# Kernel optimization log

Hardware: AMD Instinct MI355X
Metric: run time of the kernel (lower is better)

## Reference

```python
import jax, jax.numpy as jnp
import numpy as np

B, S, D, E, H, K = 2, 2048, 1024, 8, 2048, 2
EM_ITERS = 5
LB_WEIGHT = 0.1
EPS = 1e-8


def setup_inputs() -> dict:
    key = jax.random.key(0)
    ks = jax.random.split(key, 12)
    sc = 0.02
    return {
        "x": jax.random.normal(ks[0], (B, S, D), jnp.float32),
        "gate_W": jax.random.normal(ks[1], (D, E), jnp.float32) * sc,
        "gate_b": jnp.zeros((E,), jnp.float32),
        "gate_temp": jnp.ones((1,), jnp.float32),
        "W1": jax.random.normal(ks[2], (E, D, H), jnp.float32) * sc,
        "b1": jnp.zeros((E, H), jnp.float32),
        "W2": jax.random.normal(ks[3], (E, H, D), jnp.float32) * sc,
        "b2": jnp.zeros((E, D), jnp.float32),
        "sW1": jax.random.normal(ks[4], (D, H), jnp.float32) * sc,
        "sb1": jnp.zeros((H,), jnp.float32),
        "sW2": jax.random.normal(ks[5], (H, D), jnp.float32) * sc,
        "sb2": jnp.zeros((D,), jnp.float32),
    }


def reference(x, gate_W, gate_b, gate_temp, W1, b1, W2, b2, sW1, sb1, sW2, sb2):
    Bq, Sq, Dq = x.shape
    T = Bq * Sq
    xf = x.reshape(T, Dq)  # (T, D)

    # Router: gate linear + learned temperature
    gate_logits = xf @ gate_W + gate_b              # (T, E)
    tempered = gate_logits / gate_temp               # (T, E)
    expert_weights = jax.nn.softmax(tempered, axis=-1)
    _, topk_idx = jax.lax.top_k(expert_weights, K)   # (T, K) int32
    first = topk_idx[:, 0]

    # Load-balance loss: KL(uniform || empirical top-1 usage) (fresh counters)
    usage = jnp.zeros((E,), jnp.float32).at[first].add(1.0)
    actual = usage / jnp.float32(T)
    actual = actual + EPS
    actual = actual / actual.sum()
    u = jnp.float32(1.0 / E)
    kl = jnp.sum(u * (jnp.log(u) - jnp.log(actual)))
    load_balance_loss = LB_WEIGHT * kl

    # EM expert-load reweighting on tempered logits
    scores = jax.nn.softmax(tempered, axis=-1)       # (T, E)
    p = jnp.full((E,), 1.0 / E, jnp.float32)
    for _ in range(EM_ITERS):
        ea = scores * p                               # (T, E)
        ea = ea / (ea.sum(axis=-1, keepdims=True) + EPS)
        counts = ea.sum(axis=0)                       # (E,)
        p = counts / (counts.sum() + EPS)
    balanced = scores * p                             # (T, E)

    # All-expert FFN (dense, equivalent to per-expert masked compute)
    h = jax.nn.relu(jnp.einsum('td,edh->teh', xf, W1) + b1)  # (T, E, H)
    eo = jnp.einsum('teh,ehd->ted', h, W2) + b2              # (T, E, D)

    # Combine top-k experts with balanced weights
    w_k = jnp.take_along_axis(balanced, topk_idx, axis=1)        # (T, K)
    out_k = jnp.take_along_axis(eo, topk_idx[:, :, None], axis=1)  # (T, K, D)
    out = jnp.einsum('tk,tkd->td', w_k, out_k)                   # (T, D)

    # Shared expert, weighted by 0.1
    shared = jax.nn.relu(xf @ sW1 + sb1) @ sW2 + sb2
    out = out + 0.1 * shared

    return out.reshape(Bq, Sq, Dq), load_balance_loss
```

## Files before the change

kernel.cpp:

```cpp
#include <hip/hip_runtime.h>
#include <math.h>

#define T_TOK 4096
#define D_DIM 1024
#define H_DIM 2048
#define NE 8
#define EPSF 1e-8f
#define G1_GEMM 448
#define G2_GEMM 224
#define NTR128 1152

typedef __attribute__((ext_vector_type(8))) short bf16x8;
typedef __attribute__((ext_vector_type(4))) float f32x4;

__device__ __forceinline__ unsigned short f2bf(float f) {
  unsigned u = __float_as_uint(f);
  u += 0x7fffu + ((u >> 16) & 1u);
  return (unsigned short)(u >> 16);
}

__device__ __forceinline__ void gload_lds16(const void* g, void* l) {
  __builtin_amdgcn_global_load_lds(
      (const __attribute__((address_space(1))) unsigned int*)g,
      (__attribute__((address_space(3))) unsigned int*)l, 16, 0, 0);
}

#define WAITV(n) asm volatile("s_waitcnt vmcnt(" #n ")" ::: "memory")
#define BARR()                                  \
  do {                                          \
    asm volatile("" ::: "memory");              \
    __builtin_amdgcn_s_barrier();               \
    asm volatile("" ::: "memory");              \
  } while (0)

__device__ __forceinline__ void transpose_tile128(const float* __restrict__ src,
                                                  unsigned short* __restrict__ dst,
                                                  int R, int C, int r0, int c0, int tid,
                                                  float* tile) {
#pragma unroll
  for (int k = 0; k < 8; ++k) {
    int id = tid + k * 512;
    int row = id >> 5, c4 = (id & 31) * 4;
    float4 v = *(const float4*)(src + (size_t)(r0 + row) * C + c0 + c4);
    float* tr = tile + row * 129 + c4;
    tr[0] = v.x; tr[1] = v.y; tr[2] = v.z; tr[3] = v.w;
  }
  __syncthreads();
#pragma unroll
  for (int k = 0; k < 4; ++k) {
    int id = tid + k * 512;
    int oc = id >> 4;
    int rbase = (id & 15) * 8;
    uint4 wv;
    unsigned* wp = (unsigned*)&wv;
#pragma unroll
    for (int j = 0; j < 4; ++j) {
      unsigned lo = f2bf(tile[(rbase + 2 * j) * 129 + oc]);
      unsigned hi = f2bf(tile[(rbase + 2 * j + 1) * 129 + oc]);
      wp[j] = lo | (hi << 16);
    }
    *(uint4*)(dst + (size_t)(c0 + oc) * R + r0 + rbase) = wv;
  }
}

__global__ __launch_bounds__(512, 4) void prep2_kernel(
    const float* __restrict__ x, const float* __restrict__ gW, const float* __restrict__ gb,
    const float* __restrict__ gtemp, const float* __restrict__ W1, const float* __restrict__ sW1,
    unsigned short* __restrict__ W1t, unsigned short* __restrict__ sW1t,
    unsigned short* __restrict__ xb, float* __restrict__ scores, int* __restrict__ idx,
    unsigned* __restrict__ usage, unsigned* __restrict__ cnt, int* __restrict__ perm) {
  __shared__ char psm[67584];
  int b = blockIdx.x, tid = threadIdx.x;
  if (b >= 512) {
    int l = b - 512;
    int m = l >> 7, rem = l & 127;
    int c0 = (rem & 15) * 128, r0 = (rem >> 4) * 128;
    const float* src = (m < NE) ? W1 + (size_t)m * D_DIM * H_DIM : sW1;
    unsigned short* dst = (m < NE) ? W1t + (size_t)m * D_DIM * H_DIM : sW1t;
    transpose_tile128(src, dst, D_DIM, H_DIM, r0, c0, tid, (float*)psm);
    return;
  }
  float* gWl = (float*)psm;
  int* toks = (int*)(psm + 36864);
  int wave = tid >> 6, lane = tid & 63;
  int t0 = b * 8;
#pragma unroll
  for (int k = 0; k < 4; ++k) {
    int q = tid + k * 512;
    float4 f = ((const float4*)gW)[q];
    int d = q >> 1, eo = (q & 1) * 4;
    float* dstv = &gWl[d * 9 + eo];
    dstv[0] = f.x; dstv[1] = f.y; dstv[2] = f.z; dstv[3] = f.w;
  }
  __syncthreads();
  int t = t0 + wave;
  const float* xr = x + (size_t)t * D_DIM;
  unsigned short* xbr = xb + (size_t)t * D_DIM;
  float part[NE];
#pragma unroll
  for (int e = 0; e < NE; ++e) part[e] = 0.f;
#pragma unroll
  for (int i = 0; i < 16; ++i) {
    int d = lane + 64 * i;
    float xv = xr[d];
    xbr[d] = f2bf(xv);
    const float* g = &gWl[d * 9];
#pragma unroll
    for (int e = 0; e < NE; ++e) part[e] += xv * g[e];
  }
#pragma unroll
  for (int e = 0; e < NE; ++e) {
    float v = part[e];
    for (int off = 32; off; off >>= 1) v += __shfl_xor(v, off);
    part[e] = v;
  }
  float temp = gtemp[0];
  float mx = -1e30f;
#pragma unroll
  for (int e = 0; e < NE; ++e) { part[e] = (part[e] + gb[e]) / temp; mx = fmaxf(mx, part[e]); }
  float s = 0.f;
#pragma unroll
  for (int e = 0; e < NE; ++e) { part[e] = expf(part[e] - mx); s += part[e]; }
  float inv = 1.0f / s;
#pragma unroll
  for (int e = 0; e < NE; ++e) part[e] *= inv;
  if (lane == 0) {
    float4* sp = (float4*)(scores + (size_t)t * NE);
    sp[0] = make_float4(part[0], part[1], part[2], part[3]);
    sp[1] = make_float4(part[4], part[5], part[6], part[7]);
    int i0 = 0; float b0 = part[0];
#pragma unroll
    for (int e = 1; e < NE; ++e) if (part[e] > b0) { b0 = part[e]; i0 = e; }
    int i1 = -1; float b1 = -1e30f;
#pragma unroll
    for (int e = 0; e < NE; ++e) if (e != i0 && part[e] > b1) { b1 = part[e]; i1 = e; }
    idx[t * 2] = i0; idx[t * 2 + 1] = i1;
    toks[wave * 2] = i0; toks[wave * 2 + 1] = i1;
  }
  __syncthreads();
  if (tid < NE) {
    int c0 = 0, c1 = 0;
#pragma unroll
    for (int j = 0; j < 8; ++j) {
      if (toks[j * 2] == tid) ++c0;
      if (toks[j * 2 + 1] == tid) ++c1;
    }
    if (c0) atomicAdd(&usage[tid], (unsigned)c0);
    int tot = c0 + c1;
    if (tot) {
      unsigned bb = atomicAdd(&cnt[tid], (unsigned)tot);
      int p = 0;
#pragma unroll
      for (int j = 0; j < 8; ++j) {
        if (toks[j * 2] == tid) perm[(size_t)tid * T_TOK + bb + p++] = (t0 + j) * 2;
        if (toks[j * 2 + 1] == tid) perm[(size_t)tid * T_TOK + bb + p++] = (t0 + j) * 2 + 1;
      }
    }
  }
}

__device__ __forceinline__ void em_block512(const float* __restrict__ scores,
                                            const unsigned* __restrict__ usage,
                                            float* __restrict__ p_out, float* __restrict__ loss_out,
                                            int tid, char* smem) {
  float* p_sh = (float*)smem;
  float* cw = p_sh + 8;
  float* counts_sh = cw + 64;
  int wave = tid >> 6, lane = tid & 63;
  float s[8][NE];
#pragma unroll
  for (int rr = 0; rr < 8; ++rr) {
    int row = tid + rr * 512;
    const float4* sp = (const float4*)(scores + (size_t)row * NE);
    float4 a = sp[0], b = sp[1];
    s[rr][0] = a.x; s[rr][1] = a.y; s[rr][2] = a.z; s[rr][3] = a.w;
    s[rr][4] = b.x; s[rr][5] = b.y; s[rr][6] = b.z; s[rr][7] = b.w;
  }
  if (tid < NE) p_sh[tid] = 1.0f / NE;
  __syncthreads();
  for (int it = 0; it < 5; ++it) {
    float p[NE];
#pragma unroll
    for (int e = 0; e < NE; ++e) p[e] = p_sh[e];
    float c[NE];
#pragma unroll
    for (int e = 0; e < NE; ++e) c[e] = 0.f;
#pragma unroll
    for (int rr = 0; rr < 8; ++rr) {
      float denom = 0.f;
#pragma unroll
      for (int e = 0; e < NE; ++e) denom += s[rr][e] * p[e];
      float inv = 1.0f / (denom + EPSF);
#pragma unroll
      for (int e = 0; e < NE; ++e) c[e] += s[rr][e] * p[e] * inv;
    }
#pragma unroll
    for (int e = 0; e < NE; ++e) {
      float v = c[e];
      for (int off = 32; off; off >>= 1) v += __shfl_xor(v, off);
      c[e] = v;
    }
    if (lane == 0) {
#pragma unroll
      for (int e = 0; e < NE; ++e) cw[wave * 8 + e] = c[e];
    }
    __syncthreads();
    if (tid < NE) {
      float tot = 0.f;
#pragma unroll
      for (int w = 0; w < 8; ++w) tot += cw[w * 8 + tid];
      counts_sh[tid] = tot;
    }
    __syncthreads();
    if (tid < NE) {
      float total = 0.f;
#pragma unroll
      for (int e = 0; e < NE; ++e) total += counts_sh[e];
      p_sh[tid] = counts_sh[tid] / (total + EPSF);
    }
    __syncthreads();
  }
  if (tid < NE) p_out[tid] = p_sh[tid];
  if (tid == 0) {
    float actual[NE]; float norm = 0.f;
#pragma unroll
    for (int e = 0; e < NE; ++e) { actual[e] = (float)usage[e] / (float)T_TOK + EPSF; norm += actual[e]; }
    float u = 1.0f / NE;
    float kl = 0.f;
#pragma unroll
    for (int e = 0; e < NE; ++e) kl += u * (logf(u) - logf(actual[e] / norm));
    loss_out[0] = 0.1f * kl;
  }
}

template <int KDIM, int NDIM, bool RELU, bool MODE1>
__device__ __forceinline__ void gemm_body(
    unsigned short* lds, int flat,
    const unsigned short* __restrict__ A, const unsigned short* __restrict__ WE,
    const unsigned short* __restrict__ WS, const float* __restrict__ biasE,
    const float* __restrict__ biasS, const int* __restrict__ perm,
    const unsigned* __restrict__ cnt, void* __restrict__ outp) {
  constexpr int BM = 256, BN = 256, BK = 64;
  constexpr int NT = NDIM / BN;
  constexpr int NKT = KDIM / BK;

  int tc[9];
#pragma unroll
  for (int i = 0; i < NE; ++i) tc[i] = ((int)cnt[i] + 255) >> 8;
  tc[8] = T_TOK / 256;
  int nt = 0;
#pragma unroll
  for (int i = 0; i < 9; ++i) nt += tc[i];
  int W = nt * NT;
  int xcd = flat & 7, pos = flat >> 3;
  int q = W >> 3, r = W & 7;
  int mycount = q + (xcd < r ? 1 : 0);
  if (pos >= mycount) return;
  int mystart = xcd * q + (xcd < r ? xcd : r);
  int w = mystart + pos;
  int ti = w / NT;
  int n0 = (w % NT) * BN;
  int e = 0, mt = ti;
  while (mt >= tc[e]) { mt -= tc[e]; ++e; }
  int m0 = mt * BM;
  int cnt_e = (e == NE) ? T_TOK : (int)cnt[e];

  const unsigned short* Bmat = (e == NE) ? WS : WE + (size_t)e * KDIM * NDIM;
  const float* bias = (e == NE) ? biasS : biasE + (size_t)e * NDIM;

  int tid = threadIdx.x, wave = tid >> 6, lane = tid & 63;
  int wm = wave >> 1, wn = wave & 1;
  int frow = lane & 15, fks = lane >> 4;

  int srow = wave * 8 + (lane >> 3);
  int sslot = lane & 7;
  const unsigned short* aptr[2][2];
  const unsigned short* bptr[2][2];
#pragma unroll
  for (int h = 0; h < 2; ++h)
#pragma unroll
    for (int j = 0; j < 2; ++j) {
      int rr = h * 128 + j * 64 + srow;
      int colsw = (sslot ^ (rr & 7)) << 3;
      int ar = m0 + rr;
      if (ar > cnt_e - 1) ar = cnt_e - 1;
      int gar;
      if (e == NE) gar = MODE1 ? ar : (2 * T_TOK + ar);
      else { int v = perm[(size_t)e * T_TOK + ar]; gar = MODE1 ? (v >> 1) : v; }
      aptr[h][j] = A + (size_t)gar * KDIM + colsw;
      bptr[h][j] = Bmat + (size_t)(n0 + rr) * KDIM + colsw;
    }

  auto stA = [&](int t, int h) {
    int dbe = (t & 1) * 16384;
    int k0 = t * BK;
    gload_lds16(aptr[h][0] + k0, &lds[dbe + h * 8192 + wave * 512]);
    gload_lds16(aptr[h][1] + k0, &lds[dbe + h * 8192 + wave * 512 + 4096]);
  };
  auto stB = [&](int t, int h) {
    int dbe = (t & 1) * 16384;
    int k0 = t * BK;
    gload_lds16(bptr[h][0] + k0, &lds[32768 + dbe + h * 8192 + wave * 512]);
    gload_lds16(bptr[h][1] + k0, &lds[32768 + dbe + h * 8192 + wave * 512 + 4096]);
  };

  auto rdA = [&](int dbe, int ks, int m) -> bf16x8 {
    int rr = wm * 64 + m * 16 + frow;
    int slot = (ks * 4 + fks) ^ (rr & 7);
    return *(const bf16x8*)&lds[dbe + rr * 64 + slot * 8];
  };
  auto rdB = [&](int dbe, int ks, int bh, int jj) -> bf16x8 {
    int rr = bh * 128 + jj * 32 + wn * 16 + frow;
    int slot = (ks * 4 + fks) ^ (rr & 7);
    return *(const bf16x8*)&lds[32768 + dbe + rr * 64 + slot * 8];
  };

  f32x4 acc[4][8];
#pragma unroll
  for (int m = 0; m < 4; ++m)
#pragma unroll
    for (int nn = 0; nn < 8; ++nn) acc[m][nn] = (f32x4){0.f, 0.f, 0.f, 0.f};

  stA(0, 0); stA(0, 1);
  stB(0, 0); stB(0, 1);
  stA(1, 0); stA(1, 1);
  WAITV(4);
  BARR();

  for (int t = 0; t < NKT; ++t) {
    const int dbe = (t & 1) * 16384;
    bf16x8 a0[4], a1[4], b0[4], b1[4];

#pragma unroll
    for (int m = 0; m < 4; ++m) a0[m] = rdA(dbe, 0, m);
#pragma unroll
    for (int m = 0; m < 4; ++m) a1[m] = rdA(dbe, 1, m);
#pragma unroll
    for (int jj = 0; jj < 4; ++jj) b0[jj] = rdB(dbe, 0, 0, jj);
#pragma unroll
    for (int jj = 0; jj < 4; ++jj) b1[jj] = rdB(dbe, 1, 0, jj);
    if (t + 1 < NKT) { stB(t + 1, 0); stB(t + 1, 1); }
    BARR();
    __builtin_amdgcn_s_setprio(1);
#pragma unroll
    for (int m = 0; m < 4; ++m)
#pragma unroll
      for (int jj = 0; jj < 4; ++jj)
        acc[m][jj] = __builtin_amdgcn_mfma_f32_16x16x32_bf16(a0[m], b0[jj], acc[m][jj], 0, 0, 0);
#pragma unroll
    for (int m = 0; m < 4; ++m)
#pragma unroll
      for (int jj = 0; jj < 4; ++jj)
        acc[m][jj] = __builtin_amdgcn_mfma_f32_16x16x32_bf16(a1[m], b1[jj], acc[m][jj], 0, 0, 0);
    __builtin_amdgcn_s_setprio(0);
    BARR();

#pragma unroll
    for (int jj = 0; jj < 4; ++jj) b0[jj] = rdB(dbe, 0, 1, jj);
#pragma unroll
    for (int jj = 0; jj < 4; ++jj) b1[jj] = rdB(dbe, 1, 1, jj);
    if (t + 2 < NKT) { stA(t + 2, 0); stA(t + 2, 1); }
    BARR();
    __builtin_amdgcn_s_setprio(1);
#pragma unroll
    for (int m = 0; m < 4; ++m)
#pragma unroll
      for (int jj = 0; jj < 4; ++jj)
        acc[m][4 + jj] = __builtin_amdgcn_mfma_f32_16x16x32_bf16(a0[m], b0[jj], acc[m][4 + jj], 0, 0, 0);
#pragma unroll
    for (int m = 0; m < 4; ++m)
#pragma unroll
      for (int jj = 0; jj < 4; ++jj)
        acc[m][4 + jj] = __builtin_amdgcn_mfma_f32_16x16x32_bf16(a1[m], b1[jj], acc[m][4 + jj], 0, 0, 0);
    __builtin_amdgcn_s_setprio(0);
    if (t + 2 < NKT) { WAITV(4); }
    else if (t + 1 < NKT) { WAITV(0); }
    BARR();
  }

#pragma unroll
  for (int m = 0; m < 4; ++m) {
#pragma unroll
    for (int qq = 0; qq < 4; ++qq) {
      int rt = wm * 64 + m * 16 + (lane >> 4) * 4 + qq;
      if (m0 + rt >= cnt_e) continue;
      int rr;
      if (e == NE) rr = 2 * T_TOK + m0 + rt;
      else rr = perm[(size_t)e * T_TOK + m0 + rt];
#pragma unroll
      for (int nn = 0; nn < 8; ++nn) {
        int col = n0 + (nn >> 2) * 128 + (nn & 3) * 32 + wn * 16 + (lane & 15);
        float val = acc[m][nn][qq] + bias[col];
        if (RELU) val = fmaxf(val, 0.f);
        if (MODE1)
          ((unsigned short*)outp)[(size_t)rr * NDIM + col] = f2bf(val);
        else
          ((float*)outp)[(size_t)rr * NDIM + col] = val;
      }
    }
  }
}

__global__ __launch_bounds__(512, 2) void gemm1_kernel(
    const unsigned short* __restrict__ xb, const unsigned short* __restrict__ W1t,
    const unsigned short* __restrict__ sW1t, const float* __restrict__ b1,
    const float* __restrict__ sb1, const int* __restrict__ perm, const unsigned* __restrict__ cnt,
    unsigned short* __restrict__ Hbuf,
    const float* __restrict__ W2, const float* __restrict__ sW2,
    unsigned short* __restrict__ W2t, unsigned short* __restrict__ sW2t,
    const float* __restrict__ scores, const unsigned* __restrict__ usage,
    float* __restrict__ pbuf, float* __restrict__ loss_out) {
  __shared__ char smem[131072];
  int flat = blockIdx.x;
  if (flat < G1_GEMM) {
    gemm_body<D_DIM, H_DIM, true, true>((unsigned short*)smem, flat, xb, W1t, sW1t, b1, sb1,
                                        perm, cnt, (void*)Hbuf);
    return;
  }
  int l = flat - G1_GEMM;
  if (l < NTR128) {
    int m = l >> 7, rem = l & 127;
    int c0 = (rem & 7) * 128, r0 = (rem >> 3) * 128;
    const float* src = (m < NE) ? W2 + (size_t)m * H_DIM * D_DIM : sW2;
    unsigned short* dst = (m < NE) ? W2t + (size_t)m * H_DIM * D_DIM : sW2t;
    transpose_tile128(src, dst, H_DIM, D_DIM, r0, c0, threadIdx.x, (float*)smem);
    return;
  }
  em_block512(scores, usage, pbuf, loss_out, threadIdx.x, smem);
}

template <int KDIM, int NDIM, bool RELU, bool MODE1>
__global__ __launch_bounds__(512, 2) void gemm_kernel(
    const unsigned short* __restrict__ A, const unsigned short* __restrict__ WE,
    const unsigned short* __restrict__ WS, const float* __restrict__ biasE,
    const float* __restrict__ biasS, const int* __restrict__ perm,
    const unsigned* __restrict__ cnt, void* __restrict__ outp) {
  __shared__ char smem[131072];
  gemm_body<KDIM, NDIM, RELU, MODE1>((unsigned short*)smem, blockIdx.x, A, WE, WS, biasE, biasS,
                                     perm, cnt, outp);
}

__global__ void combine_kernel(const float* __restrict__ ebuf, const float* __restrict__ scores,
                               const float* __restrict__ p, const int* __restrict__ idx,
                               float* __restrict__ out) {
  int gid = blockIdx.x * blockDim.x + threadIdx.x;
  int t = gid >> 8;
  int d4 = gid & 255;
  int e0 = idx[t * 2], e1 = idx[t * 2 + 1];
  float w0 = scores[(size_t)t * NE + e0] * p[e0];
  float w1 = scores[(size_t)t * NE + e1] * p[e1];
  const float4* r0 = (const float4*)(ebuf + (size_t)(t * 2) * D_DIM);
  const float4* r1 = (const float4*)(ebuf + (size_t)(t * 2 + 1) * D_DIM);
  const float4* rs = (const float4*)(ebuf + (size_t)(2 * T_TOK + t) * D_DIM);
  float4 a = r0[d4], b = r1[d4], c = rs[d4];
  float4 o;
  o.x = w0 * a.x + w1 * b.x + 0.1f * c.x;
  o.y = w0 * a.y + w1 * b.y + 0.1f * c.y;
  o.z = w0 * a.z + w1 * b.z + 0.1f * c.z;
  o.w = w0 * a.w + w1 * b.w + 0.1f * c.w;
  ((float4*)out)[gid] = o;
}

extern "C" void kernel_launch(void* const* d_in, const int* in_sizes, int n_in,
                              void* d_out, int out_size, void* d_ws, size_t ws_size,
                              hipStream_t stream) {
  const float* x     = (const float*)d_in[0];
  const float* gW    = (const float*)d_in[1];
  const float* gb    = (const float*)d_in[2];
  const float* gtemp = (const float*)d_in[3];
  const float* W1    = (const float*)d_in[4];
  const float* b1    = (const float*)d_in[5];
  const float* W2    = (const float*)d_in[6];
  const float* b2    = (const float*)d_in[7];
  const float* sW1   = (const float*)d_in[8];
  const float* sb1   = (const float*)d_in[9];
  const float* sW2   = (const float*)d_in[10];
  const float* sb2   = (const float*)d_in[11];
  float* out = (float*)d_out;

  char* ws = (char*)d_ws;
  size_t off = 0;
  auto take = [&](size_t b) { char* ptr = ws + off; off += (b + 255) & ~(size_t)255; return ptr; };
  unsigned short* xb   = (unsigned short*)take((size_t)T_TOK * D_DIM * 2);
  unsigned short* W1t  = (unsigned short*)take((size_t)NE * H_DIM * D_DIM * 2);
  unsigned short* sW1t = (unsigned short*)take((size_t)H_DIM * D_DIM * 2);
  unsigned short* W2t  = (unsigned short*)take((size_t)NE * D_DIM * H_DIM * 2);
  unsigned short* sW2t = (unsigned short*)take((size_t)D_DIM * H_DIM * 2);
  unsigned short* Hbuf = (unsigned short*)take((size_t)3 * T_TOK * H_DIM * 2);
  float* ebuf          = (float*)take((size_t)3 * T_TOK * D_DIM * 4);
  float* scores        = (float*)take((size_t)T_TOK * NE * 4);
  int* idx             = (int*)take((size_t)T_TOK * 2 * 4);
  int* perm            = (int*)take((size_t)NE * T_TOK * 4);
  unsigned* cnt        = (unsigned*)take(256);
  unsigned* usage      = (unsigned*)take(256);
  float* pbuf          = (float*)take(256);
  (void)n_in; (void)in_sizes; (void)out_size; (void)ws_size;

  hipMemsetAsync(cnt, 0, 512, stream);
  prep2_kernel<<<512 + NTR128, 512, 0, stream>>>(x, gW, gb, gtemp, W1, sW1, W1t, sW1t, xb,
                                                 scores, idx, usage, cnt, perm);
  gemm1_kernel<<<G1_GEMM + NTR128 + 1, 512, 0, stream>>>(
      xb, W1t, sW1t, b1, sb1, perm, cnt, Hbuf, W2, sW2, W2t, sW2t, scores, usage, pbuf,
      out + (size_t)T_TOK * D_DIM);
  gemm_kernel<H_DIM, D_DIM, false, false><<<G2_GEMM, 512, 0, stream>>>(
      Hbuf, W2t, sW2t, b2, sb2, perm, cnt, (void*)ebuf);
  combine_kernel<<<(T_TOK * D_DIM / 4) / 256, 256, 0, stream>>>(ebuf, scores, pbuf, idx, out);
}
```

Before: 196.3 us.

## Fuse MoE pipeline into persistent ticketed megakernel with fine-grained dataflow sync

```diff
diff --git a/kernel.cpp b/kernel.cpp
--- a/kernel.cpp
+++ b/kernel.cpp
@@ -6,9 +6,26 @@
 #define H_DIM 2048
 #define NE 8
 #define EPSF 1e-8f
-#define G1_GEMM 448
-#define G2_GEMM 224
-#define NTR128 1152
+
+#define NT1 8
+#define NT2 4
+#define OFF_W1 512
+#define N_W1 1152
+#define OFF_G1 (OFF_W1 + N_W1)
+#define N_G1 448
+#define OFF_W2 (OFF_G1 + N_G1)
+#define N_W2 1152
+#define OFF_EM (OFF_W2 + N_W2)
+#define OFF_G2 (OFF_EM + 1)
+#define N_G2 448
+#define N_TICKETS (OFF_G2 + N_G2)
+#define HROWS 14336
+
+#define S_Q 0
+#define S_GATE 1
+#define S_W1B 2
+#define S_HB (S_W1B + 72)
+#define S_W2B (S_HB + 144)
 
 typedef __attribute__((ext_vector_type(8))) short bf16x8;
 typedef __attribute__((ext_vector_type(4))) float f32x4;
@@ -33,6 +50,23 @@
     asm volatile("" ::: "memory");              \
   } while (0)
 
+__device__ __forceinline__ unsigned ld_cnt(const unsigned* p) {
+  return __hip_atomic_load(p, __ATOMIC_RELAXED, __HIP_MEMORY_SCOPE_AGENT);
+}
+
+__device__ __forceinline__ void block_signal(unsigned* ctr, int tid) {
+  __syncthreads();
+  if (tid == 0) __hip_atomic_fetch_add(ctr, 1u, __ATOMIC_RELEASE, __HIP_MEMORY_SCOPE_AGENT);
+}
+
+__device__ __forceinline__ void block_wait(const unsigned* ctr, unsigned tgt, int tid) {
+  if (tid == 0) {
+    while (__hip_atomic_load(ctr, __ATOMIC_ACQUIRE, __HIP_MEMORY_SCOPE_AGENT) < tgt)
+      __builtin_amdgcn_s_sleep(16);
+  }
+  __syncthreads();
+}
+
 __device__ __forceinline__ void transpose_tile128(const float* __restrict__ src,
                                                   unsigned short* __restrict__ dst,
                                                   int R, int C, int r0, int c0, int tid,
@@ -63,100 +97,29 @@
   }
 }
 
-__global__ __launch_bounds__(512, 4) void prep2_kernel(
-    const float* __restrict__ x, const float* __restrict__ gW, const float* __restrict__ gb,
-    const float* __restrict__ gtemp, const float* __restrict__ W1, const float* __restrict__ sW1,
-    unsigned short* __restrict__ W1t, unsigned short* __restrict__ sW1t,
-    unsigned short* __restrict__ xb, float* __restrict__ scores, int* __restrict__ idx,
-    unsigned* __restrict__ usage, unsigned* __restrict__ cnt, int* __restrict__ perm) {
-  __shared__ char psm[67584];
-  int b = blockIdx.x, tid = threadIdx.x;
-  if (b >= 512) {
-    int l = b - 512;
-    int m = l >> 7, rem = l & 127;
-    int c0 = (rem & 15) * 128, r0 = (rem >> 4) * 128;
-    const float* src = (m < NE) ? W1 + (size_t)m * D_DIM * H_DIM : sW1;
-    unsigned short* dst = (m < NE) ? W1t + (size_t)m * D_DIM * H_DIM : sW1t;
-    transpose_tile128(src, dst, D_DIM, H_DIM, r0, c0, tid, (float*)psm);
-    return;
-  }
-  float* gWl = (float*)psm;
-  int* toks = (int*)(psm + 36864);
-  int wave = tid >> 6, lane = tid & 63;
-  int t0 = b * 8;
-#pragma unroll
-  for (int k = 0; k < 4; ++k) {
-    int q = tid + k * 512;
-    float4 f = ((const float4*)gW)[q];
-    int d = q >> 1, eo = (q & 1) * 4;
-    float* dstv = &gWl[d * 9 + eo];
-    dstv[0] = f.x; dstv[1] = f.y; dstv[2] = f.z; dstv[3] = f.w;
-  }
-  __syncthreads();
-  int t = t0 + wave;
-  const float* xr = x + (size_t)t * D_DIM;
-  unsigned short* xbr = xb + (size_t)t * D_DIM;
-  float part[NE];
-#pragma unroll
-  for (int e = 0; e < NE; ++e) part[e] = 0.f;
-#pragma unroll
-  for (int i = 0; i < 16; ++i) {
-    int d = lane + 64 * i;
-    float xv = xr[d];
-    xbr[d] = f2bf(xv);
-    const float* g = &gWl[d * 9];
-#pragma unroll
-    for (int e = 0; e < NE; ++e) part[e] += xv * g[e];
-  }
-#pragma unroll
-  for (int e = 0; e < NE; ++e) {
-    float v = part[e];
-    for (int off = 32; off; off >>= 1) v += __shfl_xor(v, off);
-    part[e] = v;
-  }
-  float temp = gtemp[0];
-  float mx = -1e30f;
-#pragma unroll
-  for (int e = 0; e < NE; ++e) { part[e] = (part[e] + gb[e]) / temp; mx = fmaxf(mx, part[e]); }
-  float s = 0.f;
-#pragma unroll
-  for (int e = 0; e < NE; ++e) { part[e] = expf(part[e] - mx); s += part[e]; }
-  float inv = 1.0f / s;
-#pragma unroll
-  for (int e = 0; e < NE; ++e) part[e] *= inv;
-  if (lane == 0) {
-    float4* sp = (float4*)(scores + (size_t)t * NE);
-    sp[0] = make_float4(part[0], part[1], part[2], part[3]);
-    sp[1] = make_float4(part[4], part[5], part[6], part[7]);
-    int i0 = 0; float b0 = part[0];
-#pragma unroll
-    for (int e = 1; e < NE; ++e) if (part[e] > b0) { b0 = part[e]; i0 = e; }
-    int i1 = -1; float b1 = -1e30f;
-#pragma unroll
-    for (int e = 0; e < NE; ++e) if (e != i0 && part[e] > b1) { b1 = part[e]; i1 = e; }
-    idx[t * 2] = i0; idx[t * 2 + 1] = i1;
-    toks[wave * 2] = i0; toks[wave * 2 + 1] = i1;
-  }
-  __syncthreads();
-  if (tid < NE) {
-    int c0 = 0, c1 = 0;
-#pragma unroll
-    for (int j = 0; j < 8; ++j) {
-      if (toks[j * 2] == tid) ++c0;
-      if (toks[j * 2 + 1] == tid) ++c1;
-    }
-    if (c0) atomicAdd(&usage[tid], (unsigned)c0);
-    int tot = c0 + c1;
-    if (tot) {
-      unsigned bb = atomicAdd(&cnt[tid], (unsigned)tot);
-      int p = 0;
-#pragma unroll
-      for (int j = 0; j < 8; ++j) {
-        if (toks[j * 2] == tid) perm[(size_t)tid * T_TOK + bb + p++] = (t0 + j) * 2;
-        if (toks[j * 2 + 1] == tid) perm[(size_t)tid * T_TOK + bb + p++] = (t0 + j) * 2 + 1;
-      }
-    }
-  }
+struct TI { int e, mt, n0, pbase, cnt_e; };
+
+template <int NT>
+__device__ __forceinline__ bool decode_tile(const unsigned* cnt, int w, TI& o) {
+  int tc[9];
+  int nt = 0;
+#pragma unroll
+  for (int i = 0; i < NE; ++i) { tc[i] = ((int)ld_cnt(&cnt[i]) + 255) >> 8; nt += tc[i]; }
+  tc[8] = T_TOK / 256; nt += tc[8];
+  int W = nt * NT;
+  int xcd = w & 7, pos = w >> 3;
+  int q = W >> 3, r = W & 7;
+  int myc = q + (xcd < r ? 1 : 0);
+  if (pos >= myc) return false;
+  int start = xcd * q + (xcd < r ? xcd : r);
+  int ww = start + pos;
+  int ti = ww / NT;
+  o.n0 = (ww % NT) * 256;
+  int e = 0, mt = ti, pb = 0;
+  while (mt >= tc[e]) { mt -= tc[e]; pb += tc[e] * 256; ++e; }
+  o.e = e; o.mt = mt; o.pbase = pb;
+  o.cnt_e = (e == NE) ? T_TOK : (int)ld_cnt(&cnt[e]);
+  return true;
 }
 
 __device__ __forceinline__ void em_block512(const float* __restrict__ scores,
@@ -233,40 +196,14 @@
   }
 }
 
-template <int KDIM, int NDIM, bool RELU, bool MODE1>
+template <int NDIM, int ASTR, int BSTR, bool RELU, bool GATHER>
 __device__ __forceinline__ void gemm_body(
-    unsigned short* lds, int flat,
-    const unsigned short* __restrict__ A, const unsigned short* __restrict__ WE,
-    const unsigned short* __restrict__ WS, const float* __restrict__ biasE,
-    const float* __restrict__ biasS, const int* __restrict__ perm,
-    const unsigned* __restrict__ cnt, void* __restrict__ outp) {
-  constexpr int BM = 256, BN = 256, BK = 64;
-  constexpr int NT = NDIM / BN;
-  constexpr int NKT = KDIM / BK;
-
-  int tc[9];
-#pragma unroll
-  for (int i = 0; i < NE; ++i) tc[i] = ((int)cnt[i] + 255) >> 8;
-  tc[8] = T_TOK / 256;
-  int nt = 0;
-#pragma unroll
-  for (int i = 0; i < 9; ++i) nt += tc[i];
-  int W = nt * NT;
-  int xcd = flat & 7, pos = flat >> 3;
-  int q = W >> 3, r = W & 7;
-  int mycount = q + (xcd < r ? 1 : 0);
-  if (pos >= mycount) return;
-  int mystart = xcd * q + (xcd < r ? xcd : r);
-  int w = mystart + pos;
-  int ti = w / NT;
-  int n0 = (w % NT) * BN;
-  int e = 0, mt = ti;
-  while (mt >= tc[e]) { mt -= tc[e]; ++e; }
-  int m0 = mt * BM;
-  int cnt_e = (e == NE) ? T_TOK : (int)cnt[e];
-
-  const unsigned short* Bmat = (e == NE) ? WS : WE + (size_t)e * KDIM * NDIM;
-  const float* bias = (e == NE) ? biasS : biasE + (size_t)e * NDIM;
+    unsigned short* lds, int e, int m0, int n0, int cnt_e, int pbase,
+    const unsigned short* __restrict__ A, const unsigned short* __restrict__ Bmat,
+    const float* __restrict__ bias, const int* __restrict__ perm,
+    void* __restrict__ outp) {
+  constexpr int BK = 64;
+  constexpr int NKT = 1024 / BK;
 
   int tid = threadIdx.x, wave = tid >> 6, lane = tid & 63;
   int wm = wave >> 1, wn = wave & 1;
@@ -285,10 +222,10 @@
       int ar = m0 + rr;
       if (ar > cnt_e - 1) ar = cnt_e - 1;
       int gar;
-      if (e == NE) gar = MODE1 ? ar : (2 * T_TOK + ar);
-      else { int v = perm[(size_t)e * T_TOK + ar]; gar = MODE1 ? (v >> 1) : v; }
-      aptr[h][j] = A + (size_t)gar * KDIM + colsw;
-      bptr[h][j] = Bmat + (size_t)(n0 + rr) * KDIM + colsw;
+      if (GATHER) gar = (e == NE) ? ar : (perm[(size_t)e * T_TOK + ar] >> 1);
+      else gar = pbase + ar;
+      aptr[h][j] = A + (size_t)gar * ASTR + colsw;
+      bptr[h][j] = Bmat + (size_t)(n0 + rr) * BSTR + colsw;
     }
 
   auto stA = [&](int t, int h) {
@@ -384,80 +321,223 @@
     for (int qq = 0; qq < 4; ++qq) {
       int rt = wm * 64 + m * 16 + (lane >> 4) * 4 + qq;
       if (m0 + rt >= cnt_e) continue;
-      int rr;
-      if (e == NE) rr = 2 * T_TOK + m0 + rt;
-      else rr = perm[(size_t)e * T_TOK + m0 + rt];
+      size_t orow = (size_t)(pbase + m0 + rt);
 #pragma unroll
       for (int nn = 0; nn < 8; ++nn) {
         int col = n0 + (nn >> 2) * 128 + (nn & 3) * 32 + wn * 16 + (lane & 15);
-        float val = acc[m][nn][qq] + bias[col];
+        float val = acc[m][nn][qq] + (bias ? bias[col] : 0.f);
         if (RELU) val = fmaxf(val, 0.f);
-        if (MODE1)
-          ((unsigned short*)outp)[(size_t)rr * NDIM + col] = f2bf(val);
+        if (RELU)
+          ((unsigned short*)outp)[orow * NDIM + col] = f2bf(val);
         else
-          ((float*)outp)[(size_t)rr * NDIM + col] = val;
+          ((float*)outp)[orow * NDIM + col] = val;
       }
     }
   }
 }
 
-__global__ __launch_bounds__(512, 2) void gemm1_kernel(
-    const unsigned short* __restrict__ xb, const unsigned short* __restrict__ W1t,
-    const unsigned short* __restrict__ sW1t, const float* __restrict__ b1,
-    const float* __restrict__ sb1, const int* __restrict__ perm, const unsigned* __restrict__ cnt,
-    unsigned short* __restrict__ Hbuf,
+__global__ __launch_bounds__(512, 2) void mega_kernel(
+    const float* __restrict__ x, const float* __restrict__ gW, const float* __restrict__ gb,
+    const float* __restrict__ gtemp,
+    const float* __restrict__ W1, const float* __restrict__ sW1,
     const float* __restrict__ W2, const float* __restrict__ sW2,
-    unsigned short* __restrict__ W2t, unsigned short* __restrict__ sW2t,
-    const float* __restrict__ scores, const unsigned* __restrict__ usage,
-    float* __restrict__ pbuf, float* __restrict__ loss_out) {
+    const float* __restrict__ b1, const float* __restrict__ sb1,
+    const float* __restrict__ b2, const float* __restrict__ sb2,
+    unsigned short* __restrict__ xb, unsigned short* __restrict__ W1t,
+    unsigned short* __restrict__ sW1t, unsigned short* __restrict__ W2t,
+    unsigned short* __restrict__ sW2t, unsigned short* __restrict__ Hbuf,
+    float* __restrict__ eA, float* __restrict__ eB,
+    float* __restrict__ scores, int* __restrict__ idx, int* __restrict__ inv,
+    unsigned* __restrict__ usage, unsigned* __restrict__ cnt, int* __restrict__ perm,
+    unsigned* __restrict__ sync, float* __restrict__ pbuf, float* __restrict__ loss_out) {
   __shared__ char smem[131072];
-  int flat = blockIdx.x;
-  if (flat < G1_GEMM) {
-    gemm_body<D_DIM, H_DIM, true, true>((unsigned short*)smem, flat, xb, W1t, sW1t, b1, sb1,
-                                        perm, cnt, (void*)Hbuf);
+  __shared__ int tk_sh;
+  int tid = threadIdx.x;
+  if (tid == 0) tk_sh = (int)atomicAdd(&sync[S_Q], 1u);
+  __syncthreads();
+  int tk = tk_sh;
+
+  if (tk < OFF_W1) {
+    float* gWl = (float*)smem;
+    int* toks = (int*)(smem + 36864);
+    int wave = tid >> 6, lane = tid & 63;
+    int t0 = tk * 8;
+#pragma unroll
+    for (int k = 0; k < 4; ++k) {
+      int qq = tid + k * 512;
+      float4 f = ((const float4*)gW)[qq];
+      int d = qq >> 1, eo = (qq & 1) * 4;
+      float* dstv = &gWl[d * 9 + eo];
+      dstv[0] = f.x; dstv[1] = f.y; dstv[2] = f.z; dstv[3] = f.w;
+    }
+    __syncthreads();
+    int t = t0 + wave;
+    const float* xr = x + (size_t)t * D_DIM;
+    unsigned short* xbr = xb + (size_t)t * D_DIM;
+    float part[NE];
+#pragma unroll
+    for (int e = 0; e < NE; ++e) part[e] = 0.f;
+#pragma unroll
+    for (int i = 0; i < 16; ++i) {
+      int d = lane + 64 * i;
+      float xv = xr[d];
+      xbr[d] = f2bf(xv);
+      const float* g = &gWl[d * 9];
+#pragma unroll
+      for (int e = 0; e < NE; ++e) part[e] += xv * g[e];
+    }
+#pragma unroll
+    for (int e = 0; e < NE; ++e) {
+      float v = part[e];
+      for (int off = 32; off; off >>= 1) v += __shfl_xor(v, off);
+      part[e] = v;
+    }
+    float temp = gtemp[0];
+    float mx = -1e30f;
+#pragma unroll
+    for (int e = 0; e < NE; ++e) { part[e] = (part[e] + gb[e]) / temp; mx = fmaxf(mx, part[e]); }
+    float s = 0.f;
+#pragma unroll
+    for (int e = 0; e < NE; ++e) { part[e] = expf(part[e] - mx); s += part[e]; }
+    float invs = 1.0f / s;
+#pragma unroll
+    for (int e = 0; e < NE; ++e) part[e] *= invs;
+    if (lane == 0) {
+      float4* sp = (float4*)(scores + (size_t)t * NE);
+      sp[0] = make_float4(part[0], part[1], part[2], part[3]);
+      sp[1] = make_float4(part[4], part[5], part[6], part[7]);
+      int i0 = 0; float bb0 = part[0];
+#pragma unroll
+      for (int e = 1; e < NE; ++e) if (part[e] > bb0) { bb0 = part[e]; i0 = e; }
+      int i1 = -1; float bb1 = -1e30f;
+#pragma unroll
+      for (int e = 0; e < NE; ++e) if (e != i0 && part[e] > bb1) { bb1 = part[e]; i1 = e; }
+      idx[t * 2] = i0; idx[t * 2 + 1] = i1;
+      toks[wave * 2] = i0; toks[wave * 2 + 1] = i1;
+    }
+    __syncthreads();
+    if (tid < NE) {
+      int c0 = 0, c1 = 0;
+#pragma unroll
+      for (int j = 0; j < 8; ++j) {
+        if (toks[j * 2] == tid) ++c0;
+        if (toks[j * 2 + 1] == tid) ++c1;
+      }
+      if (c0) atomicAdd(&usage[tid], (unsigned)c0);
+      int tot = c0 + c1;
+      if (tot) {
+        unsigned bb = atomicAdd(&cnt[tid], (unsigned)tot);
+        int p = 0;
+#pragma unroll
+        for (int j = 0; j < 8; ++j) {
+          if (toks[j * 2] == tid) {
+            perm[(size_t)tid * T_TOK + bb + p] = (t0 + j) * 2;
+            inv[(t0 + j) * 2] = (int)bb + p; ++p;
+          }
+          if (toks[j * 2 + 1] == tid) {
+            perm[(size_t)tid * T_TOK + bb + p] = (t0 + j) * 2 + 1;
+            inv[(t0 + j) * 2 + 1] = (int)bb + p; ++p;
+          }
+        }
+      }
+    }
+    block_signal(&sync[S_GATE], tid);
     return;
   }
-  int l = flat - G1_GEMM;
-  if (l < NTR128) {
+
+  if (tk < OFF_G1) {
+    int l = tk - OFF_W1;
+    int m = l >> 7, rem = l & 127;
+    int c0 = (rem & 15) * 128, r0 = (rem >> 4) * 128;
+    const float* src = (m < NE) ? W1 + (size_t)m * D_DIM * H_DIM : sW1;
+    unsigned short* dst = (m < NE) ? W1t + (size_t)m * D_DIM * H_DIM : sW1t;
+    transpose_tile128(src, dst, D_DIM, H_DIM, r0, c0, tid, (float*)smem);
+    block_signal(&sync[S_W1B + m * 8 + (c0 >> 8)], tid);
+    return;
+  }
+
+  if (tk < OFF_W2) {
+    block_wait(&sync[S_GATE], 512, tid);
+    TI ti;
+    if (!decode_tile<NT1>(cnt, tk - OFF_G1, ti)) return;
+    block_wait(&sync[S_W1B + ti.e * 8 + (ti.n0 >> 8)], 16, tid);
+    const unsigned short* Bm = (ti.e == NE) ? sW1t : W1t + (size_t)ti.e * D_DIM * H_DIM;
+    const float* bias = (ti.e == NE) ? sb1 : b1 + (size_t)ti.e * H_DIM;
+    gemm_body<H_DIM, D_DIM, D_DIM, true, true>((unsigned short*)smem, ti.e, ti.mt * 256, ti.n0,
+                                               ti.cnt_e, ti.pbase, xb, Bm, bias, perm,
+                                               (void*)Hbuf);
+    block_signal(&sync[S_HB + ti.e * 16 + ti.mt], tid);
+    return;
+  }
+
+  if (tk < OFF_EM) {
+    int l = tk - OFF_W2;
     int m = l >> 7, rem = l & 127;
     int c0 = (rem & 7) * 128, r0 = (rem >> 3) * 128;
     const float* src = (m < NE) ? W2 + (size_t)m * H_DIM * D_DIM : sW2;
     unsigned short* dst = (m < NE) ? W2t + (size_t)m * H_DIM * D_DIM : sW2t;
-    transpose_tile128(src, dst, H_DIM, D_DIM, r0, c0, threadIdx.x, (float*)smem);
+    transpose_tile128(src, dst, H_DIM, D_DIM, r0, c0, tid, (float*)smem);
+    block_signal(&sync[S_W2B + m * 4 + (c0 >> 8)], tid);
     return;
   }
-  em_block512(scores, usage, pbuf, loss_out, threadIdx.x, smem);
-}
-
-template <int KDIM, int NDIM, bool RELU, bool MODE1>
-__global__ __launch_bounds__(512, 2) void gemm_kernel(
-    const unsigned short* __restrict__ A, const unsigned short* __restrict__ WE,
-    const unsigned short* __restrict__ WS, const float* __restrict__ biasE,
-    const float* __restrict__ biasS, const int* __restrict__ perm,
-    const unsigned* __restrict__ cnt, void* __restrict__ outp) {
-  __shared__ char smem[131072];
-  gemm_body<KDIM, NDIM, RELU, MODE1>((unsigned short*)smem, blockIdx.x, A, WE, WS, biasE, biasS,
-                                     perm, cnt, outp);
-}
-
-__global__ void combine_kernel(const float* __restrict__ ebuf, const float* __restrict__ scores,
-                               const float* __restrict__ p, const int* __restrict__ idx,
-                               float* __restrict__ out) {
-  int gid = blockIdx.x * blockDim.x + threadIdx.x;
+
+  if (tk == OFF_EM) {
+    block_wait(&sync[S_GATE], 512, tid);
+    em_block512(scores, usage, pbuf, loss_out, tid, smem);
+    return;
+  }
+
+  if (tk < N_TICKETS) {
+    block_wait(&sync[S_GATE], 512, tid);
+    int v = tk - OFF_G2;
+    int ks = v & 1;
+    TI ti;
+    if (!decode_tile<NT2>(cnt, v >> 1, ti)) return;
+    block_wait(&sync[S_HB + ti.e * 16 + ti.mt], 8, tid);
+    block_wait(&sync[S_W2B + ti.e * 4 + (ti.n0 >> 8)], 32, tid);
+    const unsigned short* Am = Hbuf + ks * 1024;
+    const unsigned short* Bm = ((ti.e == NE) ? sW2t : W2t + (size_t)ti.e * H_DIM * D_DIM) + ks * 1024;
+    const float* bias = ks ? nullptr : ((ti.e == NE) ? sb2 : b2 + (size_t)ti.e * D_DIM);
+    float* outp = ks ? eB : eA;
+    gemm_body<D_DIM, H_DIM, H_DIM, false, false>((unsigned short*)smem, ti.e, ti.mt * 256, ti.n0,
+                                                 ti.cnt_e, ti.pbase, Am, Bm, bias, perm,
+                                                 (void*)outp);
+    return;
+  }
+}
+
+__global__ __launch_bounds__(256) void combine_kernel(
+    const float* __restrict__ eA, const float* __restrict__ eB,
+    const float* __restrict__ scores, const float* __restrict__ p,
+    const int* __restrict__ idx, const int* __restrict__ inv,
+    const unsigned* __restrict__ cnt, float* __restrict__ out) {
+  __shared__ int bases[9];
+  int tid = threadIdx.x;
+  if (tid == 0) {
+    int pb = 0;
+    for (int e = 0; e < NE; ++e) { bases[e] = pb; pb += (((int)cnt[e] + 255) >> 8) * 256; }
+    bases[8] = pb;
+  }
+  __syncthreads();
+  int gid = blockIdx.x * 256 + tid;
   int t = gid >> 8;
   int d4 = gid & 255;
   int e0 = idx[t * 2], e1 = idx[t * 2 + 1];
+  size_t r0 = (size_t)(bases[e0] + inv[t * 2]) * 256 + d4;
+  size_t r1 = (size_t)(bases[e1] + inv[t * 2 + 1]) * 256 + d4;
+  size_t rs = (size_t)(bases[8] + t) * 256 + d4;
   float w0 = scores[(size_t)t * NE + e0] * p[e0];
   float w1 = scores[(size_t)t * NE + e1] * p[e1];
-  const float4* r0 = (const float4*)(ebuf + (size_t)(t * 2) * D_DIM);
-  const float4* r1 = (const float4*)(ebuf + (size_t)(t * 2 + 1) * D_DIM);
-  const float4* rs = (const float4*)(ebuf + (size_t)(2 * T_TOK + t) * D_DIM);
-  float4 a = r0[d4], b = r1[d4], c = rs[d4];
+  const float4* A4 = (const float4*)eA;
+  const float4* B4 = (const float4*)eB;
+  float4 a0 = A4[r0], b0 = B4[r0];
+  float4 a1 = A4[r1], b1 = B4[r1];
+  float4 as = A4[rs], bs = B4[rs];
   float4 o;
-  o.x = w0 * a.x + w1 * b.x + 0.1f * c.x;
-  o.y = w0 * a.y + w1 * b.y + 0.1f * c.y;
-  o.z = w0 * a.z + w1 * b.z + 0.1f * c.z;
-  o.w = w0 * a.w + w1 * b.w + 0.1f * c.w;
+  o.x = w0 * (a0.x + b0.x) + w1 * (a1.x + b1.x) + 0.1f * (as.x + bs.x);
+  o.y = w0 * (a0.y + b0.y) + w1 * (a1.y + b1.y) + 0.1f * (as.y + bs.y);
+  o.z = w0 * (a0.z + b0.z) + w1 * (a1.z + b1.z) + 0.1f * (as.z + bs.z);
+  o.w = w0 * (a0.w + b0.w) + w1 * (a1.w + b1.w) + 0.1f * (as.w + bs.w);
   ((float4*)out)[gid] = o;
 }
 
@@ -486,23 +566,24 @@
   unsigned short* sW1t = (unsigned short*)take((size_t)H_DIM * D_DIM * 2);
   unsigned short* W2t  = (unsigned short*)take((size_t)NE * D_DIM * H_DIM * 2);
   unsigned short* sW2t = (unsigned short*)take((size_t)D_DIM * H_DIM * 2);
-  unsigned short* Hbuf = (unsigned short*)take((size_t)3 * T_TOK * H_DIM * 2);
-  float* ebuf          = (float*)take((size_t)3 * T_TOK * D_DIM * 4);
+  unsigned short* Hbuf = (unsigned short*)take((size_t)HROWS * H_DIM * 2);
+  float* eA            = (float*)take((size_t)HROWS * D_DIM * 4);
+  float* eB            = (float*)take((size_t)HROWS * D_DIM * 4);
   float* scores        = (float*)take((size_t)T_TOK * NE * 4);
   int* idx             = (int*)take((size_t)T_TOK * 2 * 4);
+  int* inv             = (int*)take((size_t)T_TOK * 2 * 4);
   int* perm            = (int*)take((size_t)NE * T_TOK * 4);
   unsigned* cnt        = (unsigned*)take(256);
   unsigned* usage      = (unsigned*)take(256);
+  unsigned* syncb      = (unsigned*)take(4096);
   float* pbuf          = (float*)take(256);
   (void)n_in; (void)in_sizes; (void)out_size; (void)ws_size;
 
-  hipMemsetAsync(cnt, 0, 512, stream);
-  prep2_kernel<<<512 + NTR128, 512, 0, stream>>>(x, gW, gb, gtemp, W1, sW1, W1t, sW1t, xb,
-                                                 scores, idx, usage, cnt, perm);
-  gemm1_kernel<<<G1_GEMM + NTR128 + 1, 512, 0, stream>>>(
-      xb, W1t, sW1t, b1, sb1, perm, cnt, Hbuf, W2, sW2, W2t, sW2t, scores, usage, pbuf,
-      out + (size_t)T_TOK * D_DIM);
-  gemm_kernel<H_DIM, D_DIM, false, false><<<G2_GEMM, 512, 0, stream>>>(
-      Hbuf, W2t, sW2t, b2, sb2, perm, cnt, (void*)ebuf);
-  combine_kernel<<<(T_TOK * D_DIM / 4) / 256, 256, 0, stream>>>(ebuf, scores, pbuf, idx, out);
-}
+  hipMemsetAsync(cnt, 0, 256 + 256 + 4096, stream);
+  mega_kernel<<<N_TICKETS, 512, 0, stream>>>(
+      x, gW, gb, gtemp, W1, sW1, W2, sW2, b1, sb1, b2, sb2,
+      xb, W1t, sW1t, W2t, sW2t, Hbuf, eA, eB,
+      scores, idx, inv, usage, cnt, perm, syncb, pbuf, out + (size_t)T_TOK * D_DIM);
+  combine_kernel<<<(T_TOK * D_DIM / 4) / 256, 256, 0, stream>>>(
+      eA, eB, scores, pbuf, idx, inv, cnt, out);
+}
```

After: 397.2 us. 2.02x slower.
